# Performance work log

Hardware: AMD Instinct MI355X
Metric: run time of the kernel (lower is better)

The kernel has to match this reference:

```python
import jax, jax.numpy as jnp
import numpy as np

# --- config (matches init_kwargs) ---
HID = 2048      # hidden_size
H = 16          # num_attention_heads
D_NOPE = 128    # qk_nope_head_dim
D_ROPE = 64     # qk_rope_head_dim
D_Q = D_NOPE + D_ROPE  # 192
D_V = 128       # v_head_dim
QR = 1536       # q_lora_rank
KVR = 512       # kv_lora_rank
PH = 16         # pattern_heads
PD = HID // PH  # 128
THETA = 10000.0
EPS = 1e-6


def rmsnorm(x, w):
    var = jnp.mean(jnp.square(x), axis=-1, keepdims=True)
    return x * jax.lax.rsqrt(var + EPS) * w


def rope_cos_sin(seq_len):
    inv_freq = 1.0 / (THETA ** (jnp.arange(0, D_ROPE, 2, dtype=jnp.float32) / D_ROPE))
    t = jnp.arange(seq_len, dtype=jnp.float32)
    freqs = jnp.outer(t, inv_freq)            # [S, D_ROPE/2]
    emb = jnp.concatenate([freqs, freqs], -1)  # [S, D_ROPE]
    return jnp.cos(emb), jnp.sin(emb)


def rotate_half(x):
    x1, x2 = jnp.split(x, 2, axis=-1)
    return jnp.concatenate([-x2, x1], axis=-1)


def apply_rope(x, cos, sin):
    # x: [B, H, S, D_ROPE]; cos/sin: [S, D_ROPE]
    return x * cos[None, None] + rotate_half(x) * sin[None, None]


def setup_inputs() -> dict:
    key = jax.random.key(0)
    ks = jax.random.split(key, 12)
    def w(k, shape):
        return (jax.random.normal(k, shape, jnp.float32) / np.sqrt(shape[-1])).astype(jnp.float32)
    B, S = 2, 1024
    return {
        "hidden_states": jax.random.normal(ks[0], (B, S, HID), jnp.float32),
        "q_a_w": w(ks[1], (QR, HID)),
        "q_a_ln_w": jnp.ones((QR,), jnp.float32),
        "q_b_w": w(ks[2], (H * D_Q, QR)),
        "kv_a_w": w(ks[3], (KVR + H * D_ROPE, HID)),
        "kv_a_ln_w": jnp.ones((KVR,), jnp.float32),
        "kv_b_w": w(ks[4], (H * (D_NOPE + D_V), KVR)),
        "o_w": w(ks[5], (HID, H * D_V)),
        "sp_q_w": w(ks[6], (HID, HID)),
        "sp_k_w": w(ks[7], (HID, HID)),
        "sp_v_w": w(ks[8], (HID, HID)),
        "sp_o_w": w(ks[9], (HID, HID)),
        "gate_w": w(ks[10], (2, HID)),
        "gate_b": jnp.zeros((2,), jnp.float32),
    }


def reference(hidden_states, q_a_w, q_a_ln_w, q_b_w, kv_a_w, kv_a_ln_w, kv_b_w,
              o_w, sp_q_w, sp_k_w, sp_v_w, sp_o_w, gate_w, gate_b):
    b, s, _ = hidden_states.shape
    dt = hidden_states.dtype

    # ---- main MLA path ----
    q_mid = rmsnorm(hidden_states @ q_a_w.T, q_a_ln_w)                      # [B,S,QR]
    q = (q_mid @ q_b_w.T).reshape(b, s, H, D_Q).transpose(0, 2, 1, 3)       # [B,H,S,Dq]
    q_nope, q_pe = q[..., :D_NOPE], q[..., D_NOPE:]

    kv_a = hidden_states @ kv_a_w.T                                         # [B,S,KVR+H*Dr]
    kv_lora, k_pe_flat = kv_a[..., :KVR], kv_a[..., KVR:]
    k_pe = k_pe_flat.reshape(b, s, H, D_ROPE).transpose(0, 2, 1, 3)         # [B,H,S,Dr]

    kv = (rmsnorm(kv_lora, kv_a_ln_w) @ kv_b_w.T)
    kv = kv.reshape(b, s, H, D_NOPE + D_V).transpose(0, 2, 1, 3)            # [B,H,S,Dn+Dv]
    k_nope, v = kv[..., :D_NOPE], kv[..., D_NOPE:]

    cos, sin = rope_cos_sin(s)
    q_pe = apply_rope(q_pe, cos, sin)
    k_pe = apply_rope(k_pe, cos, sin)

    qf = jnp.concatenate([q_nope, q_pe], -1)                                # [B,H,S,Dq]
    kf = jnp.concatenate([k_nope, k_pe], -1)

    scale = D_Q ** -0.5
    scores = jnp.einsum('bhqd,bhkd->bhqk', qf, kf) * scale
    probs = jax.nn.softmax(scores.astype(jnp.float32), axis=-1).astype(dt)
    ctx = jnp.einsum('bhqk,bhkd->bhqd', probs, v)                           # [B,H,S,Dv]
    main_out = ctx.transpose(0, 2, 1, 3).reshape(b, s, H * D_V) @ o_w.T     # [B,S,HID]

    # ---- self pattern path (standard MHA on hidden_states) ----
    def split_heads(x):
        return x.reshape(b, s, PH, PD).transpose(0, 2, 1, 3)
    pq = split_heads(hidden_states @ sp_q_w.T)
    pk = split_heads(hidden_states @ sp_k_w.T)
    pv = split_heads(hidden_states @ sp_v_w.T)
    p_scores = jnp.einsum('bhqd,bhkd->bhqk', pq, pk) * (PD ** -0.5)
    p_probs = jax.nn.softmax(p_scores.astype(jnp.float32), axis=-1).astype(dt)
    p_ctx = jnp.einsum('bhqk,bhkd->bhqd', p_probs, pv)
    pattern_out = p_ctx.transpose(0, 2, 1, 3).reshape(b, s, HID) @ sp_o_w.T

    # ---- learned gate over paths ----
    gates = jax.nn.softmax(hidden_states @ gate_w.T + gate_b, axis=-1)      # [B,S,2]
    return gates[..., 0:1] * main_out + gates[..., 1:2] * pattern_out
```

## Files before the change

kernel.cpp:

```cpp
#include <hip/hip_runtime.h>
#include <math.h>
#include <stdint.h>

#define HIDN  2048
#define NH    16
#define DNOPE 128
#define DROPE 64
#define DQ    192
#define DV    128
#define QRANK 1536
#define KVRANK 512
#define SEQ   1024
#define NBATCH 2
#define NTOK  (NBATCH*SEQ)
#define EPSV  1e-6f

typedef unsigned short u16;
typedef unsigned int   u32;
typedef __attribute__((ext_vector_type(8))) short  short8;
typedef __attribute__((ext_vector_type(8))) unsigned short ushort8;
typedef __attribute__((ext_vector_type(4))) float  f32x4;

__device__ __forceinline__ u16 f2b(float f) {
    u32 u = __float_as_uint(f);
    u = (u + 0x7fffu + ((u >> 16) & 1u)) >> 16;
    return (u16)u;
}
__device__ __forceinline__ float b2f(u16 h) {
    return __uint_as_float(((u32)h) << 16);
}

__device__ __forceinline__ void async_copy16(const u16* g, u16* l) {
    __builtin_amdgcn_global_load_lds(
        (const __attribute__((address_space(1))) u32*)g,
        (__attribute__((address_space(3))) u32*)l,
        16, 0, 0);
}

__device__ __forceinline__ int swz(int r, int c) { return r * 4 + (c ^ ((r >> 1) & 3)); }

#define DPP_ROR(x, ctrl) __int_as_float(__builtin_amdgcn_update_dpp( \
    __float_as_int(x), __float_as_int(x), ctrl, 0xF, 0xF, false))

__device__ __forceinline__ float rowmax16(float x) {
    x = fmaxf(x, DPP_ROR(x, 0x121));
    x = fmaxf(x, DPP_ROR(x, 0x122));
    x = fmaxf(x, DPP_ROR(x, 0x124));
    x = fmaxf(x, DPP_ROR(x, 0x128));
    return x;
}
__device__ __forceinline__ float rowsum16(float x) {
    x += DPP_ROR(x, 0x121);
    x += DPP_ROR(x, 0x122);
    x += DPP_ROR(x, 0x124);
    x += DPP_ROR(x, 0x128);
    return x;
}

struct CastArgs {
    const float* s[10];
    u16* d[10];
    int cum[11];
};
__global__ __launch_bounds__(256)
void cast_all(CastArgs a, int total_chunks)
{
    int c = blockIdx.x * 256 + threadIdx.x;
    if (c >= total_chunks) return;
    int seg = 0;
    #pragma unroll
    for (int i = 1; i < 10; ++i) seg += (c >= a.cum[i]) ? 1 : 0;
    int local = c - a.cum[seg];
    const float* src = a.s[seg] + (size_t)local * 8;
    u16* dst = a.d[seg] + (size_t)local * 8;
    float4 x = *(const float4*)(src);
    float4 y = *(const float4*)(src + 4);
    ushort8 o;
    o[0]=f2b(x.x); o[1]=f2b(x.y); o[2]=f2b(x.z); o[3]=f2b(x.w);
    o[4]=f2b(y.x); o[5]=f2b(y.y); o[6]=f2b(y.z); o[7]=f2b(y.w);
    *(ushort8*)(dst) = o;
}

struct GemmSeg {
    const u16* X; const u16* W;
    float* Cf; u16* Cb; u16* Cb2; u16* Cb3;
    int K; int ldx; int ldc; int mode; int bx0;
};
struct GemmArgs { GemmSeg seg[3]; int nseg; };

__global__ __launch_bounds__(256)
void gemm_multi(GemmArgs a)
{
    __shared__ __align__(16) u16 As[2 * 4096];
    __shared__ __align__(16) u16 Bs[2 * 4096];
    int s = 0;
    if (a.nseg > 1 && (int)blockIdx.y >= a.seg[1].bx0) s = 1;
    if (a.nseg > 2 && (int)blockIdx.y >= a.seg[2].bx0) s = 2;
    const GemmSeg g = a.seg[s];

    const int tid = threadIdx.x;
    const int bn = ((int)blockIdx.y - g.bx0) * 128;
    const int bm = blockIdx.x * 128;
    const int lane = tid & 63, wv = tid >> 6;
    const int lm = lane & 15, lq = lane >> 4;
    const int wm = (wv >> 1) * 64, wn = (wv & 1) * 64;
    const int ldx = g.ldx, K = g.K;
    const u16* Xp = g.X;
    const u16* Wp = g.W;

    auto stage = [&](int kt, int buf) {
        int k0 = kt * 32;
        #pragma unroll
        for (int it = 0; it < 2; ++it) {
            int base = wv * 64 + it * 256;
            int slot = base + lane;
            int r = slot >> 2, c = (slot & 3) ^ ((r >> 1) & 3);
            async_copy16(Xp + (size_t)(bm + r) * ldx + k0 + c * 8,
                         As + buf * 4096 + base * 8);
            async_copy16(Wp + (size_t)(bn + r) * K + k0 + c * 8,
                         Bs + buf * 4096 + base * 8);
        }
    };

    f32x4 acc[4][4] = {};
    const int niter = K >> 5;
    stage(0, 0);
    for (int kt = 0; kt < niter; ++kt) {
        int cur = kt & 1;
        __syncthreads();
        if (kt + 1 < niter) stage(kt + 1, cur ^ 1);
        const u16* Ab = As + cur * 4096;
        const u16* Bb = Bs + cur * 4096;
        short8 af[4], bf[4];
        #pragma unroll
        for (int mt = 0; mt < 4; ++mt) {
            int R = wm + mt * 16 + lm;
            af[mt] = *(const short8*)(Ab + swz(R, lq) * 8);
        }
        #pragma unroll
        for (int nt = 0; nt < 4; ++nt) {
            int R = wn + nt * 16 + lm;
            bf[nt] = *(const short8*)(Bb + swz(R, lq) * 8);
        }
        #pragma unroll
        for (int mt = 0; mt < 4; ++mt)
            #pragma unroll
            for (int nt = 0; nt < 4; ++nt)
                acc[mt][nt] = __builtin_amdgcn_mfma_f32_16x16x32_bf16(
                    af[mt], bf[nt], acc[mt][nt], 0, 0, 0);
    }

    const int mode = g.mode;
    #pragma unroll
    for (int mt = 0; mt < 4; ++mt) {
        int token0 = bm + wm + mt * 16 + lq * 4;
        #pragma unroll
        for (int nt = 0; nt < 4; ++nt) {
            int feat = bn + wn + nt * 16 + lm;
            #pragma unroll
            for (int i = 0; i < 4; ++i) {
                float v = acc[mt][nt][i];
                int tok = token0 + i;
                int b2 = tok >> 10, s2 = tok & (SEQ - 1);
                if (mode == 0) {
                    g.Cf[(size_t)tok * g.ldc + feat] = v;
                } else if (mode == 5) {
                    g.Cb[(size_t)tok * g.ldc + feat] = f2b(v);
                } else if (mode == 1) {
                    int h2 = feat / DQ, d = feat - h2 * DQ;
                    g.Cb[((size_t)((b2 * NH + h2) * SEQ + s2)) * DQ + d] = f2b(v);
                } else if (mode == 3) {
                    int h2 = feat >> 8, c = feat & 255;
                    if (c < 128)
                        g.Cb[((size_t)((b2 * NH + h2) * SEQ + s2)) * DQ + c] = f2b(v);
                    else
                        g.Cb2[((size_t)((b2 * NH + h2) * 128 + (c - 128))) * SEQ + s2] = f2b(v);
                } else {
                    int wsel = feat >> 11;
                    int f2 = feat & 2047;
                    int h2 = f2 >> 7, d = f2 & 127;
                    if (wsel == 0)
                        g.Cb[((size_t)((b2 * NH + h2) * SEQ + s2)) * 128 + d] = f2b(v);
                    else if (wsel == 1)
                        g.Cb2[((size_t)((b2 * NH + h2) * SEQ + s2)) * 128 + d] = f2b(v);
                    else
                        g.Cb3[((size_t)((b2 * NH + h2) * 128 + d)) * SEQ + s2] = f2b(v);
                }
            }
        }
    }
}

__global__ __launch_bounds__(256)
void rmsnorm_fused(u16* __restrict__ amid, const float* __restrict__ qw,
                   const float* __restrict__ kvw)
{
    int row = blockIdx.x;
    u16* x; const float* w; int D;
    if (row < NTOK) { x = amid + (size_t)row * 3072;            w = qw;  D = QRANK; }
    else            { x = amid + (size_t)(row - NTOK) * 3072 + QRANK; w = kvw; D = KVRANK; }
    const int nc = D >> 3;
    const int tid = threadIdx.x;
    ushort8 v = {};
    float ss = 0.f;
    if (tid < nc) {
        v = *(const ushort8*)(x + tid * 8);
        #pragma unroll
        for (int j = 0; j < 8; ++j) { float f = b2f(v[j]); ss += f * f; }
    }
    __shared__ float red[256];
    red[tid] = ss;
    __syncthreads();
    for (int off = 128; off > 0; off >>= 1) {
        if (tid < off) red[tid] += red[tid + off];
        __syncthreads();
    }
    float inv = rsqrtf(red[0] / (float)D + EPSV);
    if (tid < nc) {
        float4 w0 = *(const float4*)(w + tid * 8);
        float4 w1 = *(const float4*)(w + tid * 8 + 4);
        ushort8 o;
        o[0] = f2b(b2f(v[0]) * inv * w0.x);
        o[1] = f2b(b2f(v[1]) * inv * w0.y);
        o[2] = f2b(b2f(v[2]) * inv * w0.z);
        o[3] = f2b(b2f(v[3]) * inv * w0.w);
        o[4] = f2b(b2f(v[4]) * inv * w1.x);
        o[5] = f2b(b2f(v[5]) * inv * w1.y);
        o[6] = f2b(b2f(v[6]) * inv * w1.z);
        o[7] = f2b(b2f(v[7]) * inv * w1.w);
        *(ushort8*)(x + tid * 8) = o;
    }
}

__global__ __launch_bounds__(256)
void rope_fused(u16* __restrict__ qf, const u16* __restrict__ amid,
                u16* __restrict__ kf)
{
    int t = blockIdx.x * 256 + threadIdx.x;
    bool isq = t < (1 << 20);
    int tt = isq ? t : t - (1 << 20);
    int i = tt & 31, s = (tt >> 5) & (SEQ - 1), bh = tt >> 15;
    float inv_freq = exp2f((float)i * -0.41524101186f);
    float ang = (float)s * inv_freq;
    float c, sn; sincosf(ang, &sn, &c);
    if (isq) {
        u16* p = qf + ((size_t)bh * SEQ + s) * DQ;
        float x1 = b2f(p[DNOPE + i]), x2 = b2f(p[DNOPE + 32 + i]);
        p[DNOPE + i]      = f2b(x1 * c - x2 * sn);
        p[DNOPE + 32 + i] = f2b(x2 * c + x1 * sn);
    } else {
        int h = bh & (NH - 1), bb = bh >> 4;
        const u16* src = amid + ((size_t)(bb * SEQ + s)) * 3072 + (QRANK + KVRANK) + h * DROPE;
        float x1 = b2f(src[i]), x2 = b2f(src[32 + i]);
        u16* dst = kf + ((size_t)bh * SEQ + s) * DQ + DNOPE;
        dst[i]      = f2b(x1 * c - x2 * sn);
        dst[32 + i] = f2b(x2 * c + x1 * sn);
    }
}

template<int DQK>
__device__ __forceinline__
void flash_body(const u16* __restrict__ Q, const u16* __restrict__ Kf,
                const u16* __restrict__ Vt, u16* __restrict__ ctx_out,
                float scale, u16* Ks, u16* Vs, u16* Ps, int qt, int h, int bb)
{
    constexpr int KSZ  = 32 * DQK;
    constexpr int VSZ  = 32 * 128;
    constexpr int NKIT = DQK / 64;
    constexpr int NT   = SEQ / 32;
    const int tid = threadIdx.x, lane = tid & 63, wv = tid >> 6;
    const int lm = lane & 15, lq = lane >> 4;
    const size_t bh = (size_t)bb * NH + h;
    const u16* Qb = Q + (bh * SEQ + qt * 128 + wv * 32) * (size_t)DQK;
    const u16* Kb = Kf + bh * SEQ * (size_t)DQK;
    const u16* Vb = Vt + bh * (size_t)128 * SEQ;

    short8 qfrag[2][DQK / 32];
    #pragma unroll
    for (int rh = 0; rh < 2; ++rh)
        #pragma unroll
        for (int ks = 0; ks < DQK / 32; ++ks)
            qfrag[rh][ks] = *(const short8*)(Qb + (rh * 16 + lm) * DQK + ks * 32 + lq * 8);

    auto stage = [&](int kt, int buf) {
        #pragma unroll
        for (int it = 0; it < NKIT; ++it) {
            int base = it * 256 + wv * 64;
            int slot = base + lane;
            int plane = slot >> 7, rem = slot & 127;
            int key = rem >> 2, c = (rem & 3) ^ ((key >> 1) & 3);
            async_copy16(Kb + (size_t)(kt * 32 + key) * DQK + plane * 32 + c * 8,
                         Ks + buf * KSZ + base * 8);
        }
        #pragma unroll
        for (int it = 0; it < 2; ++it) {
            int base = it * 256 + wv * 64;
            int slot = base + lane;
            int d = slot >> 2, c = (slot & 3) ^ ((d >> 1) & 3);
            async_copy16(Vb + (size_t)d * SEQ + kt * 32 + c * 8,
                         Vs + buf * VSZ + base * 8);
        }
    };

    float m_i[2][4], l_i[2][4];
    #pragma unroll
    for (int rh = 0; rh < 2; ++rh)
        #pragma unroll
        for (int i = 0; i < 4; ++i) { m_i[rh][i] = -INFINITY; l_i[rh][i] = 0.f; }
    f32x4 oacc[2][8] = {};

    stage(0, 0);
    for (int kt = 0; kt < NT; ++kt) {
        int cur = kt & 1;
        __syncthreads();
        if (kt + 1 < NT) stage(kt + 1, cur ^ 1);
        const u16* Kc = Ks + cur * KSZ;
        const u16* Vc = Vs + cur * VSZ;

        f32x4 sacc[2][2] = {};
        #pragma unroll
        for (int kb = 0; kb < 2; ++kb)
            #pragma unroll
            for (int ks = 0; ks < DQK / 32; ++ks) {
                int R = kb * 16 + lm;
                short8 kfr = *(const short8*)(Kc + ks * 1024 + swz(R, lq) * 8);
                sacc[0][kb] = __builtin_amdgcn_mfma_f32_16x16x32_bf16(
                    qfrag[0][ks], kfr, sacc[0][kb], 0, 0, 0);
                sacc[1][kb] = __builtin_amdgcn_mfma_f32_16x16x32_bf16(
                    qfrag[1][ks], kfr, sacc[1][kb], 0, 0, 0);
            }

        float p0[2][4], p1[2][4], mx[2][4];
        bool needb = false;
        #pragma unroll
        for (int rh = 0; rh < 2; ++rh)
            #pragma unroll
            for (int i = 0; i < 4; ++i) {
                float s0 = sacc[rh][0][i] * scale, s1 = sacc[rh][1][i] * scale;
                float m2 = rowmax16(fmaxf(s0, s1));
                p0[rh][i] = s0; p1[rh][i] = s1; mx[rh][i] = m2;
                needb |= (m2 > m_i[rh][i] + 8.f);
            }
        bool need = __any(needb);
        float alpha[2][4];
        if (need) {
            #pragma unroll
            for (int rh = 0; rh < 2; ++rh)
                #pragma unroll
                for (int i = 0; i < 4; ++i) {
                    float mnew = fmaxf(m_i[rh][i], mx[rh][i]);
                    alpha[rh][i] = __expf(m_i[rh][i] - mnew);
                    m_i[rh][i] = mnew;
                    l_i[rh][i] *= alpha[rh][i];
                }
        }
        #pragma unroll
        for (int rh = 0; rh < 2; ++rh)
            #pragma unroll
            for (int i = 0; i < 4; ++i) {
                p0[rh][i] = __expf(p0[rh][i] - m_i[rh][i]);
                p1[rh][i] = __expf(p1[rh][i] - m_i[rh][i]);
                l_i[rh][i] += rowsum16(p0[rh][i] + p1[rh][i]);
            }

        u16* Pw = Ps + wv * 1280;
        #pragma unroll
        for (int rh = 0; rh < 2; ++rh)
            #pragma unroll
            for (int i = 0; i < 4; ++i) {
                Pw[(rh * 16 + lq * 4 + i) * 40 + lm]      = f2b(p0[rh][i]);
                Pw[(rh * 16 + lq * 4 + i) * 40 + 16 + lm] = f2b(p1[rh][i]);
            }
        short8 pfrag0 = *(const short8*)(Pw + lm * 40 + lq * 8);
        short8 pfrag1 = *(const short8*)(Pw + (16 + lm) * 40 + lq * 8);

        if (need) {
            #pragma unroll
            for (int rh = 0; rh < 2; ++rh)
                #pragma unroll
                for (int nt = 0; nt < 8; ++nt)
                    #pragma unroll
                    for (int i = 0; i < 4; ++i) oacc[rh][nt][i] *= alpha[rh][i];
        }
        #pragma unroll
        for (int nt = 0; nt < 8; ++nt) {
            int R = nt * 16 + lm;
            short8 vfr = *(const short8*)(Vc + swz(R, lq) * 8);
            oacc[0][nt] = __builtin_amdgcn_mfma_f32_16x16x32_bf16(
                pfrag0, vfr, oacc[0][nt], 0, 0, 0);
            oacc[1][nt] = __builtin_amdgcn_mfma_f32_16x16x32_bf16(
                pfrag1, vfr, oacc[1][nt], 0, 0, 0);
        }
    }

    #pragma unroll
    for (int rh = 0; rh < 2; ++rh) {
        int s0 = qt * 128 + wv * 32 + rh * 16 + lq * 4;
        #pragma unroll
        for (int i = 0; i < 4; ++i) {
            float inv = 1.f / l_i[rh][i];
            u16* dst = ctx_out + ((size_t)(bb * SEQ + s0 + i) * NH + h) * 128;
            #pragma unroll
            for (int nt = 0; nt < 8; ++nt)
                dst[nt * 16 + lm] = f2b(oacc[rh][nt][i] * inv);
        }
    }
}

__global__ __launch_bounds__(256, 2)
void flash_fused(const u16* qf, const u16* kf, const u16* Vtg, u16* ctx,
                 const u16* pq, const u16* pk, const u16* pvt, u16* p_ctx,
                 float scale_main, float scale_pat)
{
    __shared__ __align__(16) u16 Ks[2 * 32 * DQ];
    __shared__ __align__(16) u16 Vs[2 * 32 * 128];
    __shared__ __align__(16) u16 Ps[4 * 32 * 40];
    int h = blockIdx.x, qtb = blockIdx.y, bb = blockIdx.z;
    if (qtb < 8)
        flash_body<DQ>(qf, kf, Vtg, ctx, scale_main, Ks, Vs, Ps, qtb, h, bb);
    else
        flash_body<128>(pq, pk, pvt, p_ctx, scale_pat, Ks, Vs, Ps, qtb - 8, h, bb);
}

__global__ __launch_bounds__(256)
void gate_combine(const float* __restrict__ x, const float* __restrict__ gw,
                  const float* __restrict__ gb,
                  const float* __restrict__ mo, const float* __restrict__ po,
                  float* __restrict__ out)
{
    const int tok = blockIdx.x;
    const float* xr = x + (size_t)tok * HIDN;
    float d0 = 0.f, d1 = 0.f;
    for (int i = threadIdx.x; i < HIDN; i += 256) {
        float v = xr[i];
        d0 += v * gw[i];
        d1 += v * gw[HIDN + i];
    }
    __shared__ float r0[256], r1[256];
    r0[threadIdx.x] = d0; r1[threadIdx.x] = d1;
    __syncthreads();
    for (int off = 128; off > 0; off >>= 1) {
        if (threadIdx.x < off) {
            r0[threadIdx.x] += r0[threadIdx.x + off];
            r1[threadIdx.x] += r1[threadIdx.x + off];
        }
        __syncthreads();
    }
    float l0 = r0[0] + gb[0], l1 = r1[0] + gb[1];
    float m = fmaxf(l0, l1);
    float e0 = __expf(l0 - m), e1 = __expf(l1 - m);
    float g0 = e0 / (e0 + e1), g1 = e1 / (e0 + e1);
    const float* mr = mo + (size_t)tok * HIDN;
    const float* pr = po + (size_t)tok * HIDN;
    float* orow = out + (size_t)tok * HIDN;
    for (int i = threadIdx.x; i < HIDN; i += 256)
        orow[i] = g0 * mr[i] + g1 * pr[i];
}

extern "C" void kernel_launch(void* const* d_in, const int* in_sizes, int n_in,
                              void* d_out, int out_size, void* d_ws, size_t ws_size,
                              hipStream_t stream)
{
    const float* X        = (const float*)d_in[0];
    const float* q_a_w    = (const float*)d_in[1];
    const float* q_a_ln_w = (const float*)d_in[2];
    const float* q_b_w    = (const float*)d_in[3];
    const float* kv_a_w   = (const float*)d_in[4];
    const float* kv_a_ln_w= (const float*)d_in[5];
    const float* kv_b_w   = (const float*)d_in[6];
    const float* o_w      = (const float*)d_in[7];
    const float* sp_q_w   = (const float*)d_in[8];
    const float* sp_k_w   = (const float*)d_in[9];
    const float* sp_v_w   = (const float*)d_in[10];
    const float* sp_o_w   = (const float*)d_in[11];
    const float* gate_w   = (const float*)d_in[12];
    const float* gate_b   = (const float*)d_in[13];
    float* out = (float*)d_out;

    char* p = (char*)d_ws;
    auto alloc = [&](size_t bytes) -> char* {
        char* r = p; p += (bytes + 255) & ~(size_t)255; return r;
    };
    u16* amid      = (u16*)alloc((size_t)NTOK * 3072 * 2);
    u16* Xb        = (u16*)alloc((size_t)NTOK * HIDN * 2);
    u16* aw_b      = (u16*)alloc((size_t)3072 * HIDN * 2);
    u16* q_b_wb    = (u16*)alloc((size_t)NH * DQ * QRANK * 2);
    u16* kv_b_wb   = (u16*)alloc((size_t)NH * 256 * KVRANK * 2);
    u16* o_wb      = (u16*)alloc((size_t)HIDN * HIDN * 2);
    u16* spqkv_wb  = (u16*)alloc((size_t)3 * HIDN * HIDN * 2);
    u16* sp_o_wb   = (u16*)alloc((size_t)HIDN * HIDN * 2);
    u16* qf        = (u16*)alloc((size_t)NTOK * NH * DQ * 2);
    u16* kf        = (u16*)alloc((size_t)NTOK * NH * DQ * 2);
    u16* Vtg       = (u16*)alloc((size_t)NBATCH * NH * 128 * SEQ * 2);
    u16* pq        = (u16*)alloc((size_t)NTOK * HIDN * 2);
    u16* pk        = (u16*)alloc((size_t)NTOK * HIDN * 2);
    u16* pvt    = aw_b;
    u16* ctx    = q_b_wb;
    u16* p_ctx  = spqkv_wb;
    float* patout = (float*)qf;

    dim3 blk(256);

    CastArgs ca;
    const float* srcs[10] = {X, q_a_w, kv_a_w, q_b_w, kv_b_w, o_w,
                             sp_q_w, sp_k_w, sp_v_w, sp_o_w};
    u16* dsts[10] = {Xb, aw_b, aw_b + (size_t)QRANK * HIDN, q_b_wb, kv_b_wb, o_wb,
                     spqkv_wb, spqkv_wb + (size_t)HIDN * HIDN,
                     spqkv_wb + (size_t)2 * HIDN * HIDN, sp_o_wb};
    int ns[10] = {NTOK * HIDN, QRANK * HIDN, 1536 * HIDN, NH * DQ * QRANK,
                  NH * 256 * KVRANK, HIDN * HIDN, HIDN * HIDN, HIDN * HIDN,
                  HIDN * HIDN, HIDN * HIDN};
    int cum = 0;
    for (int i = 0; i < 10; ++i) {
        ca.s[i] = srcs[i]; ca.d[i] = dsts[i];
        ca.cum[i] = cum; cum += ns[i] / 8;
    }
    ca.cum[10] = cum;
    cast_all<<<dim3((cum + 255) / 256), blk, 0, stream>>>(ca, cum);

    {
        GemmArgs ga = {};
        ga.nseg = 1;
        ga.seg[0] = {Xb, aw_b, nullptr, amid, nullptr, nullptr,
                     HIDN, HIDN, 3072, 5, 0};
        gemm_multi<<<dim3(16, 24), blk, 0, stream>>>(ga);
    }

    rmsnorm_fused<<<dim3(2 * NTOK), blk, 0, stream>>>(amid, q_a_ln_w, kv_a_ln_w);

    {
        GemmArgs ga = {};
        ga.nseg = 3;
        ga.seg[0] = {Xb, spqkv_wb, nullptr, pq, pk, pvt,
                     HIDN, HIDN, 0, 4, 0};
        ga.seg[1] = {amid, q_b_wb, nullptr, qf, nullptr, nullptr,
                     QRANK, 3072, 0, 1, 48};
        ga.seg[2] = {amid + QRANK, kv_b_wb, nullptr, kf, Vtg, nullptr,
                     KVRANK, 3072, 0, 3, 72};
        gemm_multi<<<dim3(16, 104), blk, 0, stream>>>(ga);
    }

    rope_fused<<<dim3(8192), blk, 0, stream>>>(qf, amid, kf);

    flash_fused<<<dim3(NH, 16, NBATCH), blk, 0, stream>>>(
        qf, kf, Vtg, ctx, pq, pk, pvt, p_ctx,
        1.0f / sqrtf((float)DQ), 1.0f / sqrtf(128.0f));

    {
        GemmArgs ga = {};
        ga.nseg = 2;
        ga.seg[0] = {ctx, o_wb, out, nullptr, nullptr, nullptr,
                     HIDN, HIDN, HIDN, 0, 0};
        ga.seg[1] = {p_ctx, sp_o_wb, patout, nullptr, nullptr, nullptr,
                     HIDN, HIDN, HIDN, 0, 16};
        gemm_multi<<<dim3(16, 32), blk, 0, stream>>>(ga);
    }

    gate_combine<<<dim3(NTOK), blk, 0, stream>>>(X, gate_w, gate_b, out, patout, out);
}
```

Before: 549.5 us.

## Fuse RMSNorm into GEMM epilogues and q-RoPE into q_b GEMM

Removes the standalone rmsnorm kernel. The first GEMM's epilogue now accumulates per-token sums of squares with atomics. The ln weights are folded into the bf16 copies of q_b_w and kv_b_w inside the cast kernel, and the inverse-rms scale is applied per row in the q_b and kv_b GEMM epilogues. The q-side RoPE moves into the q_b GEMM epilogue, so the rope kernel now handles only k. This drops two full passes over the intermediates, at the cost of atomics, a memset, and different rounding because normalization now happens after the GEMM.

Result: faster. 529.4 us (-3.7%).

```diff
diff --git a/kernel.cpp b/kernel.cpp
--- a/kernel.cpp
+++ b/kernel.cpp
@@ -61,6 +61,8 @@
     const float* s[10];
     u16* d[10];
     int cum[11];
+    const float* lnq;
+    const float* lnkv;
 };
 __global__ __launch_bounds__(256)
 void cast_all(CastArgs a, int total_chunks)
@@ -75,6 +77,15 @@
     u16* dst = a.d[seg] + (size_t)local * 8;
     float4 x = *(const float4*)(src);
     float4 y = *(const float4*)(src + 4);
+    if (seg == 3 || seg == 4) {
+        const float* ln = (seg == 3) ? a.lnq : a.lnkv;
+        u32 kmod = (seg == 3) ? (u32)QRANK : (u32)KVRANK;
+        u32 kb = ((u32)local * 8u) % kmod;
+        float4 w0 = *(const float4*)(ln + kb);
+        float4 w1 = *(const float4*)(ln + kb + 4);
+        x.x *= w0.x; x.y *= w0.y; x.z *= w0.z; x.w *= w0.w;
+        y.x *= w1.x; y.y *= w1.y; y.z *= w1.z; y.w *= w1.w;
+    }
     ushort8 o;
     o[0]=f2b(x.x); o[1]=f2b(x.y); o[2]=f2b(x.z); o[3]=f2b(x.w);
     o[4]=f2b(y.x); o[5]=f2b(y.y); o[6]=f2b(y.z); o[7]=f2b(y.w);
@@ -86,7 +97,7 @@
     float* Cf; u16* Cb; u16* Cb2; u16* Cb3;
     int K; int ldx; int ldc; int mode; int bx0;
 };
-struct GemmArgs { GemmSeg seg[3]; int nseg; };
+struct GemmArgs { GemmSeg seg[3]; int nseg; float* ssq; float* sskv; };
 
 __global__ __launch_bounds__(256)
 void gemm_multi(GemmArgs a)
@@ -151,25 +162,62 @@
     }
 
     const int mode = g.mode;
+    if (mode == 1) {
+        const int h2  = (bn + wn) / DQ;
+        const int hd0 = (bn + wn) % DQ;
+        const bool ropeH = (hd0 == 128);
+        float invf0 = 0.f, invf1 = 0.f;
+        if (ropeH) {
+            invf0 = exp2f((float)lm * -0.41524101186f);
+            invf1 = exp2f((float)(16 + lm) * -0.41524101186f);
+        }
+        #pragma unroll
+        for (int mt = 0; mt < 4; ++mt) {
+            int token0 = bm + wm + mt * 16 + lq * 4;
+            #pragma unroll
+            for (int i = 0; i < 4; ++i) {
+                int tok = token0 + i;
+                int b2 = tok >> 10, s2 = tok & (SEQ - 1);
+                float inv = rsqrtf(a.ssq[tok] * (1.f / QRANK) + EPSV);
+                u16* row = g.Cb + ((size_t)((b2 * NH + h2) * SEQ + s2)) * DQ + hd0;
+                if (!ropeH) {
+                    #pragma unroll
+                    for (int nt = 0; nt < 4; ++nt)
+                        row[nt * 16 + lm] = f2b(acc[mt][nt][i] * inv);
+                } else {
+                    float sn0, c0, sn1, c1;
+                    sincosf((float)s2 * invf0, &sn0, &c0);
+                    sincosf((float)s2 * invf1, &sn1, &c1);
+                    float x10 = acc[mt][0][i] * inv, x20 = acc[mt][2][i] * inv;
+                    float x11 = acc[mt][1][i] * inv, x21 = acc[mt][3][i] * inv;
+                    row[lm]          = f2b(x10 * c0 - x20 * sn0);
+                    row[32 + lm]     = f2b(x20 * c0 + x10 * sn0);
+                    row[16 + lm]     = f2b(x11 * c1 - x21 * sn1);
+                    row[48 + lm]     = f2b(x21 * c1 + x11 * sn1);
+                }
+            }
+        }
+        return;
+    }
     #pragma unroll
     for (int mt = 0; mt < 4; ++mt) {
         int token0 = bm + wm + mt * 16 + lq * 4;
         #pragma unroll
-        for (int nt = 0; nt < 4; ++nt) {
-            int feat = bn + wn + nt * 16 + lm;
-            #pragma unroll
-            for (int i = 0; i < 4; ++i) {
+        for (int i = 0; i < 4; ++i) {
+            int tok = token0 + i;
+            int b2 = tok >> 10, s2 = tok & (SEQ - 1);
+            float invkv = 1.f;
+            if (mode == 3) invkv = rsqrtf(a.sskv[tok] * (1.f / KVRANK) + EPSV);
+            #pragma unroll
+            for (int nt = 0; nt < 4; ++nt) {
+                int feat = bn + wn + nt * 16 + lm;
                 float v = acc[mt][nt][i];
-                int tok = token0 + i;
-                int b2 = tok >> 10, s2 = tok & (SEQ - 1);
                 if (mode == 0) {
                     g.Cf[(size_t)tok * g.ldc + feat] = v;
                 } else if (mode == 5) {
                     g.Cb[(size_t)tok * g.ldc + feat] = f2b(v);
-                } else if (mode == 1) {
-                    int h2 = feat / DQ, d = feat - h2 * DQ;
-                    g.Cb[((size_t)((b2 * NH + h2) * SEQ + s2)) * DQ + d] = f2b(v);
                 } else if (mode == 3) {
+                    v *= invkv;
                     int h2 = feat >> 8, c = feat & 255;
                     if (c < 128)
                         g.Cb[((size_t)((b2 * NH + h2) * SEQ + s2)) * DQ + c] = f2b(v);
@@ -189,73 +237,44 @@
             }
         }
     }
+    if (mode == 5) {
+        float* ssp = nullptr;
+        if (bn < QRANK) ssp = a.ssq;
+        else if (bn < QRANK + KVRANK) ssp = a.sskv;
+        if (ssp) {
+            #pragma unroll
+            for (int mt = 0; mt < 4; ++mt) {
+                int token0 = bm + wm + mt * 16 + lq * 4;
+                #pragma unroll
+                for (int i = 0; i < 4; ++i) {
+                    float sq = 0.f;
+                    #pragma unroll
+                    for (int nt = 0; nt < 4; ++nt) {
+                        float v = acc[mt][nt][i];
+                        sq += v * v;
+                    }
+                    sq = rowsum16(sq);
+                    if (lm == 0) atomicAdd(&ssp[token0 + i], sq);
+                }
+            }
+        }
+    }
 }
 
 __global__ __launch_bounds__(256)
-void rmsnorm_fused(u16* __restrict__ amid, const float* __restrict__ qw,
-                   const float* __restrict__ kvw)
-{
-    int row = blockIdx.x;
-    u16* x; const float* w; int D;
-    if (row < NTOK) { x = amid + (size_t)row * 3072;            w = qw;  D = QRANK; }
-    else            { x = amid + (size_t)(row - NTOK) * 3072 + QRANK; w = kvw; D = KVRANK; }
-    const int nc = D >> 3;
-    const int tid = threadIdx.x;
-    ushort8 v = {};
-    float ss = 0.f;
-    if (tid < nc) {
-        v = *(const ushort8*)(x + tid * 8);
-        #pragma unroll
-        for (int j = 0; j < 8; ++j) { float f = b2f(v[j]); ss += f * f; }
-    }
-    __shared__ float red[256];
-    red[tid] = ss;
-    __syncthreads();
-    for (int off = 128; off > 0; off >>= 1) {
-        if (tid < off) red[tid] += red[tid + off];
-        __syncthreads();
-    }
-    float inv = rsqrtf(red[0] / (float)D + EPSV);
-    if (tid < nc) {
-        float4 w0 = *(const float4*)(w + tid * 8);
-        float4 w1 = *(const float4*)(w + tid * 8 + 4);
-        ushort8 o;
-        o[0] = f2b(b2f(v[0]) * inv * w0.x);
-        o[1] = f2b(b2f(v[1]) * inv * w0.y);
-        o[2] = f2b(b2f(v[2]) * inv * w0.z);
-        o[3] = f2b(b2f(v[3]) * inv * w0.w);
-        o[4] = f2b(b2f(v[4]) * inv * w1.x);
-        o[5] = f2b(b2f(v[5]) * inv * w1.y);
-        o[6] = f2b(b2f(v[6]) * inv * w1.z);
-        o[7] = f2b(b2f(v[7]) * inv * w1.w);
-        *(ushort8*)(x + tid * 8) = o;
-    }
-}
-
-__global__ __launch_bounds__(256)
-void rope_fused(u16* __restrict__ qf, const u16* __restrict__ amid,
-                u16* __restrict__ kf)
+void rope_k(const u16* __restrict__ amid, u16* __restrict__ kf)
 {
     int t = blockIdx.x * 256 + threadIdx.x;
-    bool isq = t < (1 << 20);
-    int tt = isq ? t : t - (1 << 20);
-    int i = tt & 31, s = (tt >> 5) & (SEQ - 1), bh = tt >> 15;
+    int i = t & 31, s = (t >> 5) & (SEQ - 1), bh = t >> 15;
     float inv_freq = exp2f((float)i * -0.41524101186f);
     float ang = (float)s * inv_freq;
     float c, sn; sincosf(ang, &sn, &c);
-    if (isq) {
-        u16* p = qf + ((size_t)bh * SEQ + s) * DQ;
-        float x1 = b2f(p[DNOPE + i]), x2 = b2f(p[DNOPE + 32 + i]);
-        p[DNOPE + i]      = f2b(x1 * c - x2 * sn);
-        p[DNOPE + 32 + i] = f2b(x2 * c + x1 * sn);
-    } else {
-        int h = bh & (NH - 1), bb = bh >> 4;
-        const u16* src = amid + ((size_t)(bb * SEQ + s)) * 3072 + (QRANK + KVRANK) + h * DROPE;
-        float x1 = b2f(src[i]), x2 = b2f(src[32 + i]);
-        u16* dst = kf + ((size_t)bh * SEQ + s) * DQ + DNOPE;
-        dst[i]      = f2b(x1 * c - x2 * sn);
-        dst[32 + i] = f2b(x2 * c + x1 * sn);
-    }
+    int h = bh & (NH - 1), bb = bh >> 4;
+    const u16* src = amid + ((size_t)(bb * SEQ + s)) * 3072 + (QRANK + KVRANK) + h * DROPE;
+    float x1 = b2f(src[i]), x2 = b2f(src[32 + i]);
+    u16* dst = kf + ((size_t)bh * SEQ + s) * DQ + DNOPE;
+    dst[i]      = f2b(x1 * c - x2 * sn);
+    dst[32 + i] = f2b(x2 * c + x1 * sn);
 }
 
 template<int DQK>
@@ -494,12 +513,17 @@
     u16* Vtg       = (u16*)alloc((size_t)NBATCH * NH * 128 * SEQ * 2);
     u16* pq        = (u16*)alloc((size_t)NTOK * HIDN * 2);
     u16* pk        = (u16*)alloc((size_t)NTOK * HIDN * 2);
+    float* ssbuf   = (float*)alloc((size_t)2 * NTOK * 4);
     u16* pvt    = aw_b;
     u16* ctx    = q_b_wb;
     u16* p_ctx  = spqkv_wb;
     float* patout = (float*)qf;
+    float* ss_q  = ssbuf;
+    float* ss_kv = ssbuf + NTOK;
 
     dim3 blk(256);
+
+    hipMemsetAsync(ssbuf, 0, (size_t)2 * NTOK * 4, stream);
 
     CastArgs ca;
     const float* srcs[10] = {X, q_a_w, kv_a_w, q_b_w, kv_b_w, o_w,
@@ -516,6 +540,7 @@
         ca.cum[i] = cum; cum += ns[i] / 8;
     }
     ca.cum[10] = cum;
+    ca.lnq = q_a_ln_w; ca.lnkv = kv_a_ln_w;
     cast_all<<<dim3((cum + 255) / 256), blk, 0, stream>>>(ca, cum);
 
     {
@@ -523,10 +548,9 @@
         ga.nseg = 1;
         ga.seg[0] = {Xb, aw_b, nullptr, amid, nullptr, nullptr,
                      HIDN, HIDN, 3072, 5, 0};
+        ga.ssq = ss_q; ga.sskv = ss_kv;
         gemm_multi<<<dim3(16, 24), blk, 0, stream>>>(ga);
     }
-
-    rmsnorm_fused<<<dim3(2 * NTOK), blk, 0, stream>>>(amid, q_a_ln_w, kv_a_ln_w);
 
     {
         GemmArgs ga = {};
@@ -537,10 +561,11 @@
                      QRANK, 3072, 0, 1, 48};
         ga.seg[2] = {amid + QRANK, kv_b_wb, nullptr, kf, Vtg, nullptr,
                      KVRANK, 3072, 0, 3, 72};
+        ga.ssq = ss_q; ga.sskv = ss_kv;
         gemm_multi<<<dim3(16, 104), blk, 0, stream>>>(ga);
     }
 
-    rope_fused<<<dim3(8192), blk, 0, stream>>>(qf, amid, kf);
+    rope_k<<<dim3(4096), blk, 0, stream>>>(amid, kf);
 
     flash_fused<<<dim3(NH, 16, NBATCH), blk, 0, stream>>>(
         qf, kf, Vtg, ctx, pq, pk, pvt, p_ctx,
```
